# Kernel optimization log

Measured on AMD Instinct MI355X. Metric: run time of the kernel, lower is better.

Reference implementation:

```python
import jax, jax.numpy as jnp
import numpy as np
from jax import lax

K = 3  # AdaConv kernel_size inside conv_block


def conv2d(x, w, b, pad):
    # x: (B,C,H,W), w: (O,I,kh,kw) -> NCHW conv with symmetric padding
    y = lax.conv_general_dilated(x, w, (1, 1), [(pad, pad), (pad, pad)],
                                 dimension_numbers=('NCHW', 'OIHW', 'NCHW'))
    return y + b[None, :, None, None]


def unfold3(x):
    # nn.Unfold(kernel=3, pad=1): patches ordered channel-major then (kh,kw) row-major
    B, C, H, W = x.shape
    xp = jnp.pad(x, ((0, 0), (0, 0), (1, 1), (1, 1)))
    return jnp.stack([xp[:, :, i:i + H, j:j + W]
                      for i in range(K) for j in range(K)], axis=2)  # (B,C,9,H,W)


def adaconv(x, mask, aw_w, aw_b, mt_w, mt_b, c_w, c_b):
    # groups=1, groups_channels=out_ch in this configuration
    weight = conv2d(mask, aw_w, aw_b, pad=2)          # (B, 9, H, W)
    x = conv2d(x, c_w, c_b, pad=1)                    # (B, out_ch, H, W)
    p = unfold3(x)                                    # (B, out_ch, 9, H, W)
    out = jnp.einsum('bkhw,bckhw->bchw', weight, p)   # per-pixel adaptive conv
    mask2 = conv2d(mask, mt_w, mt_b, pad=2)
    return out, mask2


def lrelu(x):
    return jax.nn.leaky_relu(x, 0.01)


def setup_inputs() -> dict:
    key = jax.random.key(0)
    ks = jax.random.split(key, 20)
    B, Cin, Cout, Mi, Mo, H, W = 2, 64, 64, 64, 64, 256, 256
    s = 0.05
    d = {
        'x': jax.random.normal(ks[0], (B, Cin, H, W), jnp.float32),
        'mask': jax.random.normal(ks[1], (B, Mi, H, W), jnp.float32),
        # AdaConv 1 (in_ch->out_ch, mask_in->mask_out)
        'aw1_w': jax.random.normal(ks[2], (K * K, Mi, 2 * K - 1, 2 * K - 1), jnp.float32) * s,
        'aw1_b': jax.random.normal(ks[3], (K * K,), jnp.float32) * s,
        'mt1_w': jax.random.normal(ks[4], (Mo, Mi, 2 * K - 1, 2 * K - 1), jnp.float32) * s,
        'mt1_b': jax.random.normal(ks[5], (Mo,), jnp.float32) * s,
        'c1_w': jax.random.normal(ks[6], (Cout, Cin, K, K), jnp.float32) * s,
        'c1_b': jax.random.normal(ks[7], (Cout,), jnp.float32) * s,
        # AdaConv 2 (out_ch->out_ch, mask_out->mask_out)
        'aw2_w': jax.random.normal(ks[8], (K * K, Mo, 2 * K - 1, 2 * K - 1), jnp.float32) * s,
        'aw2_b': jax.random.normal(ks[9], (K * K,), jnp.float32) * s,
        'mt2_w': jax.random.normal(ks[10], (Mo, Mo, 2 * K - 1, 2 * K - 1), jnp.float32) * s,
        'mt2_b': jax.random.normal(ks[11], (Mo,), jnp.float32) * s,
        'c2_w': jax.random.normal(ks[12], (Cout, Cout, K, K), jnp.float32) * s,
        'c2_b': jax.random.normal(ks[13], (Cout,), jnp.float32) * s,
        # 1x1 residual conv
        'cr_w': jax.random.normal(ks[14], (Cout, Cin, 1, 1), jnp.float32) * s,
        'cr_b': jax.random.normal(ks[15], (Cout,), jnp.float32) * s,
    }
    return d


def reference(x, mask, aw1_w, aw1_b, mt1_w, mt1_b, c1_w, c1_b,
              aw2_w, aw2_b, mt2_w, mt2_b, c2_w, c2_b, cr_w, cr_b):
    res = conv2d(x, cr_w, cr_b, pad=0)
    x, mask = adaconv(x, mask, aw1_w, aw1_b, mt1_w, mt1_b, c1_w, c1_b)
    x, mask = lrelu(x), lrelu(mask)
    x, mask = adaconv(x, mask, aw2_w, aw2_b, mt2_w, mt2_b, c2_w, c2_b)
    x, mask = lrelu(x), lrelu(mask)
    return (x + res, mask)
```

## Files before the change

### kernel.cpp

```cpp
#include <hip/hip_runtime.h>

#define HWSZ 65536
#define CCH  64

typedef __bf16 bf16x8 __attribute__((ext_vector_type(8)));
typedef __bf16 bf16x4 __attribute__((ext_vector_type(4)));
typedef float  f32x4  __attribute__((ext_vector_type(4)));

__device__ inline void gload_lds16(const void* g, void* l) {
    __builtin_amdgcn_global_load_lds(
        (const __attribute__((address_space(1))) void*)g,
        (__attribute__((address_space(3))) void*)l, 16, 0, 0);
}


__device__ void cvt_body(int cb, const float* __restrict__ src,
                         __bf16* __restrict__ dst)
{
    int p  = cb * 256 + threadIdx.x;
    int b  = p >> 16, hw = p & 65535;
    const float* sp = src + (((size_t)b * 64) << 16) + hw;
    __bf16* dp = dst + (size_t)p * 64;
    #pragma unroll
    for (int c8 = 0; c8 < 8; ++c8) {
        bf16x8 v8;
        #pragma unroll
        for (int j = 0; j < 8; ++j)
            v8[j] = (__bf16)sp[(size_t)(c8 * 8 + j) << 16];
        *(bf16x8*)(dp + c8 * 8) = v8;
    }
}

__device__ void prep3_body(int cb, const float* __restrict__ src,
                           __bf16* __restrict__ dst)
{
    int t = cb * 256 + threadIdx.x;
    if (t >= 9 * 64 * 64) return;
    int j = t & 7;
    int u = (t >> 3) % 512;
    int k = t / 4096;
    int o = u >> 3;
    int s = (u & 7) ^ (o & 7);
    int i = s * 8 + j;
    dst[t] = (__bf16)src[((size_t)o * 64 + i) * 9 + k];
}

__device__ void prepF_body(int cb, const float* __restrict__ mt,
                           const float* __restrict__ aw, __bf16* __restrict__ dst)
{
    int t = cb * 256 + threadIdx.x;
    if (t >= 25 * 96 * 64) return;
    int j = t & 7;
    int u = (t >> 3) % 768;
    int k = t / 6144;
    int r = u >> 3;
    int s = (u & 7) ^ (r & 7);
    int i = s * 8 + j;
    float v = 0.f;
    if (r < 64)      v = mt[((size_t)r * 64 + i) * 25 + k];
    else if (r < 73) v = aw[((size_t)(r - 64) * 64 + i) * 25 + k];
    dst[t] = (__bf16)v;
}

__global__ __launch_bounds__(256) void k_prep(
    const float* x, const float* mask,
    const float* c1w, const float* c2w,
    const float* mt1w, const float* aw1w,
    const float* mt2w, const float* aw2w,
    __bf16* xh, __bf16* mh,
    __bf16* wbc1, __bf16* wbc2, __bf16* wbF1, __bf16* wbF2)
{
    int bid = blockIdx.x;
    if      (bid < 512)  cvt_body(bid, x, xh);
    else if (bid < 1024) cvt_body(bid - 512, mask, mh);
    else if (bid < 1168) prep3_body(bid - 1024, c1w, wbc1);
    else if (bid < 1312) prep3_body(bid - 1168, c2w, wbc2);
    else if (bid < 1912) prepF_body(bid - 1312, mt1w, aw1w, wbF1);
    else                 prepF_body(bid - 1912, mt2w, aw2w, wbF2);
}

template<int KSZ, int MFT, int RELU, int EPI>
__global__ __launch_bounds__(256) void k_mconv(
    const __bf16* __restrict__ xh, const __bf16* __restrict__ wb,
    const float* __restrict__ bias, const float* __restrict__ bias2,
    float* __restrict__ outf, __bf16* __restrict__ outh,
    float* __restrict__ out2)
{
    constexpr int PAD   = KSZ / 2;
    constexpr int TW    = 16 + 2 * PAD;
    constexpr int NPIX  = TW * TW;
    constexpr int KK    = KSZ * KSZ;
    constexpr int SROWS = (MFT == 5) ? 96 : 64;
    constexpr int SLICE = SROWS * 128;
    constexpr int NISS  = SROWS / 32;

    __shared__ __align__(16) __bf16 lx[NPIX * 64];
    __shared__ __align__(16) __bf16 lw[2][SROWS * 64];
    __shared__ float lb[80];

    const int t    = threadIdx.x;
    const int w0   = blockIdx.x * 16, h0 = blockIdx.y * 16, b = blockIdx.z;
    const int wvv  = t >> 6;
    const int lane = t & 63;
    const int px   = lane & 15;
    const int g    = lane >> 4;

    auto STAGE = [&](int k, int buf) {
        const char* gs = (const char*)wb + (size_t)k * SLICE;
        char* lbase = (char*)lw[buf];
        #pragma unroll
        for (int r = 0; r < NISS; ++r) {
            int ub = (wvv * NISS + r) * 64;
            gload_lds16(gs + (ub + lane) * 16, lbase + ub * 16);
        }
    };

    STAGE(0, 0);
    STAGE(1, 1);

    if (t < 64) lb[t] = bias[t];
    if constexpr (MFT == 5) {
        if (t >= 64 && t < 80) lb[t] = (t - 64 < 9) ? bias2[t - 64] : 0.f;
    }

    bf16x8 zv;
    #pragma unroll
    for (int j = 0; j < 8; ++j) zv[j] = (__bf16)0.f;
    constexpr int PITER = (NPIX + 255) / 256;
    #pragma unroll
    for (int pi = 0; pi < PITER; ++pi) {
        int pix = pi * 256 + t;
        if (pix < NPIX) {
            int sy = pix / TW, sx = pix - sy * TW;
            int gy = h0 + sy - PAD, gx = w0 + sx - PAD;
            bool ok = (unsigned)gy < 256u && (unsigned)gx < 256u;
            const __bf16* src = xh + ((((size_t)b << 16) + gy * 256 + gx) << 6);
            int rowbase = pix << 7, sw = (pix & 7) << 4;
            #pragma unroll
            for (int c8 = 0; c8 < 8; ++c8) {
                bf16x8 v8 = ok ? *(const bf16x8*)(src + c8 * 8) : zv;
                *(bf16x8*)((char*)lx + rowbase + ((c8 << 4) ^ sw)) = v8;
            }
        }
    }
    __syncthreads();

    f32x4 acc[MFT][4];
    #pragma unroll
    for (int m = 0; m < MFT; ++m)
        #pragma unroll
        for (int nf = 0; nf < 4; ++nf)
            acc[m][nf] = (f32x4){0.f, 0.f, 0.f, 0.f};

    #pragma unroll
    for (int k = 0; k < KK; ++k) {
        const __bf16* lwb = lw[k & 1];
        const int dy = k / KSZ, dx = k - dy * KSZ;

        bf16x8 bfr[4][2];
        #pragma unroll
        for (int nf = 0; nf < 4; ++nf) {
            int pix = (wvv * 4 + nf + dy) * TW + (px + dx);
            int rowbase = pix << 7, sw = (pix & 7) << 4;
            #pragma unroll
            for (int ks = 0; ks < 2; ++ks)
                bfr[nf][ks] = *(const bf16x8*)((const char*)lx + rowbase + ((((ks * 4 + g) << 4)) ^ sw));
        }
        bf16x8 afr[MFT][2];
        #pragma unroll
        for (int m = 0; m < MFT; ++m) {
            int o = m * 16 + px;
            int rowbase = o << 7, sw = (o & 7) << 4;
            #pragma unroll
            for (int ks = 0; ks < 2; ++ks)
                afr[m][ks] = *(const bf16x8*)((const char*)lwb + rowbase + ((((ks * 4 + g) << 4)) ^ sw));
        }
        __builtin_amdgcn_s_setprio(1);
        #pragma unroll
        for (int m = 0; m < MFT; ++m)
            #pragma unroll
            for (int nf = 0; nf < 4; ++nf)
                #pragma unroll
                for (int ks = 0; ks < 2; ++ks)
                    acc[m][nf] = __builtin_amdgcn_mfma_f32_16x16x32_bf16(
                        afr[m][ks], bfr[nf][ks], acc[m][nf], 0, 0, 0);
        __builtin_amdgcn_s_setprio(0);

        if (k == KK - 1) break;

        asm volatile("s_waitcnt lgkmcnt(0)" ::: "memory");
        __builtin_amdgcn_sched_barrier(0);
        __builtin_amdgcn_s_barrier();
        bool issued = (k + 2 < KK);
        if (issued) {
            STAGE(k + 2, k & 1);
            if constexpr (NISS == 2) asm volatile("s_waitcnt vmcnt(2)" ::: "memory");
            else                     asm volatile("s_waitcnt vmcnt(3)" ::: "memory");
        } else {
            asm volatile("s_waitcnt vmcnt(0)" ::: "memory");
        }
        __builtin_amdgcn_sched_barrier(0);
        __builtin_amdgcn_s_barrier();
    }

    #pragma unroll
    for (int m = 0; m < MFT; ++m) {
        #pragma unroll
        for (int nf = 0; nf < 4; ++nf) {
            int row = h0 + wvv * 4 + nf, col = w0 + px;
            if (m < 4) {
                float vj[4];
                #pragma unroll
                for (int j = 0; j < 4; ++j) {
                    float v = acc[m][nf][j] + lb[m * 16 + g * 4 + j];
                    if (RELU) v = v > 0.f ? v : 0.01f * v;
                    vj[j] = v;
                }
                if constexpr (EPI == 0) {
                    bf16x4 pk;
                    #pragma unroll
                    for (int j = 0; j < 4; ++j) pk[j] = (__bf16)vj[j];
                    *(bf16x4*)(outh + ((((size_t)b << 16) + row * 256 + col) << 6)
                                    + m * 16 + g * 4) = pk;
                } else {
                    #pragma unroll
                    for (int j = 0; j < 4; ++j)
                        outf[((size_t)(b * 64 + m * 16 + g * 4 + j) << 16)
                             + row * 256 + col] = vj[j];
                }
            } else {
                #pragma unroll
                for (int j = 0; j < 4; ++j) {
                    int o2 = g * 4 + j;
                    if (o2 < 9)
                        out2[((size_t)(b * 9 + o2) << 16) + row * 256 + col]
                            = acc[m][nf][j] + lb[64 + o2];
                }
            }
        }
    }
}

__global__ __launch_bounds__(256) void k_conv1x1(
    const __bf16* __restrict__ xh, const float* __restrict__ w,
    const float* __restrict__ bias, float* __restrict__ out)
{
    __shared__ __align__(16) float lwT[4096];
    __shared__ float lb[64];
    int t = threadIdx.x;
    for (int s = t; s < 4096; s += 256) lwT[s] = w[(s & 63) * 64 + (s >> 6)];
    if (t < 64) lb[t] = bias[t];
    __syncthreads();

    int p  = blockIdx.x * 256 + t;
    int b  = p >> 16, hw = p & 65535;
    const __bf16* xp = xh + (size_t)p * 64;

    float acc[64];
    #pragma unroll
    for (int o = 0; o < 64; ++o) acc[o] = lb[o];

    #pragma unroll
    for (int c8 = 0; c8 < 8; ++c8) {
        bf16x8 v8 = *(const bf16x8*)(xp + c8 * 8);
        #pragma unroll
        for (int j = 0; j < 8; ++j) {
            float xi = (float)v8[j];
            const float4* w4 = (const float4*)&lwT[(c8 * 8 + j) * 64];
            #pragma unroll
            for (int o4 = 0; o4 < 16; ++o4) {
                float4 wv = w4[o4];
                acc[o4*4+0] += wv.x * xi;
                acc[o4*4+1] += wv.y * xi;
                acc[o4*4+2] += wv.z * xi;
                acc[o4*4+3] += wv.w * xi;
            }
        }
    }
    float* op = out + (((size_t)b * 64) << 16) + hw;
    #pragma unroll
    for (int o = 0; o < 64; ++o) op[(size_t)o << 16] = acc[o];
}

__global__ __launch_bounds__(256, 4) void k_ada1(
    const float* __restrict__ wgt, const __bf16* __restrict__ xin,
    __bf16* __restrict__ outh)
{
    int t  = threadIdx.x;
    int pg = t >> 3, c8 = t & 7;
    int p  = blockIdx.x * 32 + pg;
    int b  = p >> 16, hw = p & 65535;
    int h  = hw >> 8, wc = hw & 255;

    const float* wp = wgt + ((size_t)(b * 9) << 16) + hw;
    const __bf16* cen = xin + (size_t)p * 64 + c8 * 8;

    float wk[9];
    const __bf16* nbp[9];
    #pragma unroll
    for (int dy = 0; dy < 3; ++dy)
        #pragma unroll
        for (int dx = 0; dx < 3; ++dx) {
            int k = dy * 3 + dx;
            bool ok = ((unsigned)(h + dy - 1) < 256u) &&
                      ((unsigned)(wc + dx - 1) < 256u);
            wk[k]  = ok ? wp[(size_t)k << 16] : 0.f;
            nbp[k] = ok ? cen + ((dy - 1) * 256 + (dx - 1)) * 64 : cen;
        }

    float acc[8] = {0.f,0.f,0.f,0.f,0.f,0.f,0.f,0.f};
    #pragma unroll
    for (int k = 0; k < 9; ++k) {
        bf16x8 v8 = *(const bf16x8*)nbp[k];
        float w = wk[k];
        #pragma unroll
        for (int j = 0; j < 8; ++j) acc[j] += w * (float)v8[j];
    }

    bf16x8 o8;
    #pragma unroll
    for (int j = 0; j < 8; ++j) {
        float v = acc[j];
        o8[j] = (__bf16)(v > 0.f ? v : 0.01f * v);
    }
    *(bf16x8*)(outh + (size_t)p * 64 + c8 * 8) = o8;
}

__global__ __launch_bounds__(256, 4) void k_ada2(
    const float* __restrict__ wgt, const __bf16* __restrict__ x2h,
    float* __restrict__ outf)
{
    __shared__ float ls[32 * 65];

    int t  = threadIdx.x;
    int pg = t >> 3, c8 = t & 7;
    int p  = blockIdx.x * 32 + pg;
    int b  = p >> 16, hw = p & 65535;
    int h  = hw >> 8, wc = hw & 255;

    const float* wp = wgt + ((size_t)(b * 9) << 16) + hw;
    const __bf16* cen = x2h + (size_t)p * 64 + c8 * 8;

    float wk[9];
    const __bf16* nbp[9];
    #pragma unroll
    for (int dy = 0; dy < 3; ++dy)
        #pragma unroll
        for (int dx = 0; dx < 3; ++dx) {
            int k = dy * 3 + dx;
            bool ok = ((unsigned)(h + dy - 1) < 256u) &&
                      ((unsigned)(wc + dx - 1) < 256u);
            wk[k]  = ok ? wp[(size_t)k << 16] : 0.f;
            nbp[k] = ok ? cen + ((dy - 1) * 256 + (dx - 1)) * 64 : cen;
        }

    float acc[8] = {0.f,0.f,0.f,0.f,0.f,0.f,0.f,0.f};
    #pragma unroll
    for (int k = 0; k < 9; ++k) {
        bf16x8 v8 = *(const bf16x8*)nbp[k];
        float w = wk[k];
        #pragma unroll
        for (int j = 0; j < 8; ++j) acc[j] += w * (float)v8[j];
    }

    #pragma unroll
    for (int j = 0; j < 8; ++j) {
        float v = acc[j];
        ls[pg * 65 + c8 * 8 + j] = v > 0.f ? v : 0.01f * v;
    }
    __syncthreads();

    int pbase = blockIdx.x * 32;
    int bb    = pbase >> 16, hwb = pbase & 65535;
    int pix   = t & 31, cq = t >> 5;
    #pragma unroll
    for (int i = 0; i < 8; ++i) {
        int c = i * 8 + cq;
        float v = ls[pix * 65 + c];
        float* op = outf + ((size_t)(bb * 64 + c) << 16) + hwb + pix;
        *op = *op + v;
    }
}

extern "C" void kernel_launch(void* const* d_in, const int* in_sizes, int n_in,
                              void* d_out, int out_size, void* d_ws, size_t ws_size,
                              hipStream_t stream)
{
    const float* x     = (const float*)d_in[0];
    const float* mask  = (const float*)d_in[1];
    const float* aw1_w = (const float*)d_in[2];
    const float* aw1_b = (const float*)d_in[3];
    const float* mt1_w = (const float*)d_in[4];
    const float* mt1_b = (const float*)d_in[5];
    const float* c1_w  = (const float*)d_in[6];
    const float* c1_b  = (const float*)d_in[7];
    const float* aw2_w = (const float*)d_in[8];
    const float* aw2_b = (const float*)d_in[9];
    const float* mt2_w = (const float*)d_in[10];
    const float* mt2_b = (const float*)d_in[11];
    const float* c2_w  = (const float*)d_in[12];
    const float* c2_b  = (const float*)d_in[13];
    const float* cr_w  = (const float*)d_in[14];
    const float* cr_b  = (const float*)d_in[15];

    float* out_x = (float*)d_out;
    float* out_m = (float*)d_out + 8388608;

    float*  wgt   = (float*)d_ws;
    __bf16* xh    = (__bf16*)((char*)d_ws + 4718592);
    __bf16* mh    = (__bf16*)((char*)d_ws + 21495808);
    __bf16* x2h   = mh;
    __bf16* wbase = (__bf16*)((char*)d_ws + 38273024);
    __bf16* wb_c1 = wbase;
    __bf16* wb_c2 = wbase + 36864;
    __bf16* wb_F1 = wbase + 73728;
    __bf16* wb_F2 = wbase + 227328;

    __bf16* maska_h = (__bf16*)out_x;
    __bf16* xa_h    = (__bf16*)out_x + 8388608;
    __bf16* x1_h    = (__bf16*)out_m;

    dim3 blk(256);
    dim3 gconv(16, 16, 2);
    dim3 gpix(512);
    dim3 gada(4096);

    k_prep<<<dim3(2512), blk, 0, stream>>>(x, mask, c1_w, c2_w,
        mt1_w, aw1_w, mt2_w, aw2_w, xh, mh, wb_c1, wb_c2, wb_F1, wb_F2);

    k_mconv<5,5,1,0><<<gconv, blk, 0, stream>>>(mh, wb_F1, mt1_b, aw1_b,
                                                nullptr, maska_h, wgt);
    k_mconv<3,4,0,0><<<gconv, blk, 0, stream>>>(xh, wb_c1, c1_b, nullptr,
                                                nullptr, x1_h, nullptr);
    k_ada1<<<gada, blk, 0, stream>>>(wgt, x1_h, xa_h);
    k_mconv<5,5,1,1><<<gconv, blk, 0, stream>>>(maska_h, wb_F2, mt2_b, aw2_b,
                                                out_m, nullptr, wgt);
    k_mconv<3,4,0,0><<<gconv, blk, 0, stream>>>(xa_h, wb_c2, c2_b, nullptr,
                                                nullptr, x2h, nullptr);
    k_conv1x1<<<gpix, blk, 0, stream>>>(xh, cr_w, cr_b, out_x);
    k_ada2<<<gada, blk, 0, stream>>>(wgt, x2h, out_x);
}
```

Baseline: 193.1 us.

## Split input channels into two halves to halve LDS tile footprint

The conv kernel now processes the 64 input channels in two 32-channel passes. It re-stages the input halo tile and the per-tap weight slices for each half, and the prep kernels repack weights into a matching [ci][k][row-pair] swizzled layout. This halves the shared-memory footprint for the input tile and weight buffers, which should let more blocks run per CU. The cost is twice as many pipeline barriers and tap iterations, an extra full-tile reload with its sync, and half as many MFMAs issued per tap iteration.

```diff
diff --git a/kernel.cpp b/kernel.cpp
--- a/kernel.cpp
+++ b/kernel.cpp
@@ -35,13 +35,16 @@
                            __bf16* __restrict__ dst)
 {
     int t = cb * 256 + threadIdx.x;
-    if (t >= 9 * 64 * 64) return;
-    int j = t & 7;
-    int u = (t >> 3) % 512;
-    int k = t / 4096;
-    int o = u >> 3;
-    int s = (u & 7) ^ (o & 7);
-    int i = s * 8 + j;
+    if (t >= 2 * 9 * 2048) return;
+    int j  = t & 7;
+    int u  = (t >> 3) & 255;
+    int q  = t >> 11;
+    int k  = q % 9, ci = q / 9;
+    int r  = u >> 3;
+    int v  = (u & 7) ^ (r & 7);
+    int o  = 2 * r + (v >> 2);
+    int g  = v & 3;
+    int i  = ci * 32 + g * 8 + j;
     dst[t] = (__bf16)src[((size_t)o * 64 + i) * 9 + k];
 }
 
@@ -49,17 +52,20 @@
                            const float* __restrict__ aw, __bf16* __restrict__ dst)
 {
     int t = cb * 256 + threadIdx.x;
-    if (t >= 25 * 96 * 64) return;
-    int j = t & 7;
-    int u = (t >> 3) % 768;
-    int k = t / 6144;
-    int r = u >> 3;
-    int s = (u & 7) ^ (r & 7);
-    int i = s * 8 + j;
-    float v = 0.f;
-    if (r < 64)      v = mt[((size_t)r * 64 + i) * 25 + k];
-    else if (r < 73) v = aw[((size_t)(r - 64) * 64 + i) * 25 + k];
-    dst[t] = (__bf16)v;
+    if (t >= 2 * 25 * 3072) return;
+    int j  = t & 7;
+    int u  = (t >> 3) % 384;
+    int q  = t / 3072;
+    int k  = q % 25, ci = q / 25;
+    int r  = u >> 3;
+    int v  = (u & 7) ^ (r & 7);
+    int o  = 2 * r + (v >> 2);
+    int g  = v & 3;
+    int i  = ci * 32 + g * 8 + j;
+    float val = 0.f;
+    if (o < 64)      val = mt[((size_t)o * 64 + i) * 25 + k];
+    else if (o < 73) val = aw[((size_t)(o - 64) * 64 + i) * 25 + k];
+    dst[t] = (__bf16)val;
 }
 
 __global__ __launch_bounds__(256) void k_prep(
@@ -91,11 +97,11 @@
     constexpr int NPIX  = TW * TW;
     constexpr int KK    = KSZ * KSZ;
     constexpr int SROWS = (MFT == 5) ? 96 : 64;
-    constexpr int SLICE = SROWS * 128;
-    constexpr int NISS  = SROWS / 32;
-
-    __shared__ __align__(16) __bf16 lx[NPIX * 64];
-    __shared__ __align__(16) __bf16 lw[2][SROWS * 64];
+    constexpr int SLICE = SROWS * 64;
+    constexpr int NPIX2 = NPIX / 2;
+
+    __shared__ __align__(16) __bf16 lx[NPIX2 * 64];
+    __shared__ __align__(16) __bf16 lw[2][SROWS * 32];
     __shared__ float lb[80];
 
     const int t    = threadIdx.x;
@@ -105,45 +111,22 @@
     const int px   = lane & 15;
     const int g    = lane >> 4;
 
-    auto STAGE = [&](int k, int buf) {
-        const char* gs = (const char*)wb + (size_t)k * SLICE;
+    auto STAGE = [&](int ci, int k, int buf) {
+        const char* gs = (const char*)wb + (size_t)(ci * KK + k) * SLICE;
         char* lbase = (char*)lw[buf];
-        #pragma unroll
-        for (int r = 0; r < NISS; ++r) {
-            int ub = (wvv * NISS + r) * 64;
+        if constexpr (MFT == 5) {
+            if (wvv < 3) {
+                #pragma unroll
+                for (int r = 0; r < 2; ++r) {
+                    int ub = wvv * 128 + r * 64;
+                    gload_lds16(gs + (ub + lane) * 16, lbase + ub * 16);
+                }
+            }
+        } else {
+            int ub = wvv * 64;
             gload_lds16(gs + (ub + lane) * 16, lbase + ub * 16);
         }
     };
-
-    STAGE(0, 0);
-    STAGE(1, 1);
-
-    if (t < 64) lb[t] = bias[t];
-    if constexpr (MFT == 5) {
-        if (t >= 64 && t < 80) lb[t] = (t - 64 < 9) ? bias2[t - 64] : 0.f;
-    }
-
-    bf16x8 zv;
-    #pragma unroll
-    for (int j = 0; j < 8; ++j) zv[j] = (__bf16)0.f;
-    constexpr int PITER = (NPIX + 255) / 256;
-    #pragma unroll
-    for (int pi = 0; pi < PITER; ++pi) {
-        int pix = pi * 256 + t;
-        if (pix < NPIX) {
-            int sy = pix / TW, sx = pix - sy * TW;
-            int gy = h0 + sy - PAD, gx = w0 + sx - PAD;
-            bool ok = (unsigned)gy < 256u && (unsigned)gx < 256u;
-            const __bf16* src = xh + ((((size_t)b << 16) + gy * 256 + gx) << 6);
-            int rowbase = pix << 7, sw = (pix & 7) << 4;
-            #pragma unroll
-            for (int c8 = 0; c8 < 8; ++c8) {
-                bf16x8 v8 = ok ? *(const bf16x8*)(src + c8 * 8) : zv;
-                *(bf16x8*)((char*)lx + rowbase + ((c8 << 4) ^ sw)) = v8;
-            }
-        }
-    }
-    __syncthreads();
 
     f32x4 acc[MFT][4];
     #pragma unroll
@@ -152,55 +135,87 @@
         for (int nf = 0; nf < 4; ++nf)
             acc[m][nf] = (f32x4){0.f, 0.f, 0.f, 0.f};
 
-    #pragma unroll
-    for (int k = 0; k < KK; ++k) {
-        const __bf16* lwb = lw[k & 1];
-        const int dy = k / KSZ, dx = k - dy * KSZ;
-
-        bf16x8 bfr[4][2];
-        #pragma unroll
-        for (int nf = 0; nf < 4; ++nf) {
-            int pix = (wvv * 4 + nf + dy) * TW + (px + dx);
-            int rowbase = pix << 7, sw = (pix & 7) << 4;
+    bf16x8 zv;
+    #pragma unroll
+    for (int j = 0; j < 8; ++j) zv[j] = (__bf16)0.f;
+
+    for (int ci = 0; ci < 2; ++ci) {
+        if (ci) __syncthreads();
+        STAGE(ci, 0, 0);
+        STAGE(ci, 1, 1);
+        if (ci == 0) {
+            if (t < 64) lb[t] = bias[t];
+            if constexpr (MFT == 5) {
+                if (t >= 64 && t < 80) lb[t] = (t - 64 < 9) ? bias2[t - 64] : 0.f;
+            }
+        }
+
+        constexpr int XITER = (NPIX * 4 + 255) / 256;
+        #pragma unroll
+        for (int xi = 0; xi < XITER; ++xi) {
+            int e = xi * 256 + t;
+            if (e < NPIX * 4) {
+                int pix = e >> 2, c4 = e & 3;
+                int sy = pix / TW, sx = pix - sy * TW;
+                int gy = h0 + sy - PAD, gx = w0 + sx - PAD;
+                bool ok = (unsigned)gy < 256u && (unsigned)gx < 256u;
+                bf16x8 v8 = zv;
+                if (ok) v8 = *(const bf16x8*)(xh + ((((size_t)b << 16) + gy * 256 + gx) << 6)
+                                              + ci * 32 + c4 * 8);
+                int row = pix >> 1;
+                int off = row * 128 + (((((pix & 1) << 2) + c4) ^ (row & 7)) << 4);
+                *(bf16x8*)((char*)lx + off) = v8;
+            }
+        }
+        __syncthreads();
+
+        #pragma unroll
+        for (int k = 0; k < KK; ++k) {
+            const __bf16* lwb = lw[k & 1];
+            const int dy = k / KSZ, dx = k - dy * KSZ;
+
+            bf16x8 bfr[4];
             #pragma unroll
-            for (int ks = 0; ks < 2; ++ks)
-                bfr[nf][ks] = *(const bf16x8*)((const char*)lx + rowbase + ((((ks * 4 + g) << 4)) ^ sw));
-        }
-        bf16x8 afr[MFT][2];
-        #pragma unroll
-        for (int m = 0; m < MFT; ++m) {
-            int o = m * 16 + px;
-            int rowbase = o << 7, sw = (o & 7) << 4;
+            for (int nf = 0; nf < 4; ++nf) {
+                int pix = (wvv * 4 + nf + dy) * TW + (px + dx);
+                int row = pix >> 1;
+                int off = row * 128 + (((((pix & 1) << 2) + g) ^ (row & 7)) << 4);
+                bfr[nf] = *(const bf16x8*)((const char*)lx + off);
+            }
+            bf16x8 afr[MFT];
             #pragma unroll
-            for (int ks = 0; ks < 2; ++ks)
-                afr[m][ks] = *(const bf16x8*)((const char*)lwb + rowbase + ((((ks * 4 + g) << 4)) ^ sw));
-        }
-        __builtin_amdgcn_s_setprio(1);
-        #pragma unroll
-        for (int m = 0; m < MFT; ++m)
+            for (int m = 0; m < MFT; ++m) {
+                int o = m * 16 + px;
+                int row = o >> 1;
+                int off = row * 128 + (((((o & 1) << 2) + g) ^ (row & 7)) << 4);
+                afr[m] = *(const bf16x8*)((const char*)lwb + off);
+            }
+            __builtin_amdgcn_s_setprio(1);
             #pragma unroll
-            for (int nf = 0; nf < 4; ++nf)
+            for (int m = 0; m < MFT; ++m)
                 #pragma unroll
-                for (int ks = 0; ks < 2; ++ks)
+                for (int nf = 0; nf < 4; ++nf)
                     acc[m][nf] = __builtin_amdgcn_mfma_f32_16x16x32_bf16(
-                        afr[m][ks], bfr[nf][ks], acc[m][nf], 0, 0, 0);
-        __builtin_amdgcn_s_setprio(0);
-
-        if (k == KK - 1) break;
-
-        asm volatile("s_waitcnt lgkmcnt(0)" ::: "memory");
-        __builtin_amdgcn_sched_barrier(0);
-        __builtin_amdgcn_s_barrier();
-        bool issued = (k + 2 < KK);
-        if (issued) {
-            STAGE(k + 2, k & 1);
-            if constexpr (NISS == 2) asm volatile("s_waitcnt vmcnt(2)" ::: "memory");
-            else                     asm volatile("s_waitcnt vmcnt(3)" ::: "memory");
-        } else {
-            asm volatile("s_waitcnt vmcnt(0)" ::: "memory");
-        }
-        __builtin_amdgcn_sched_barrier(0);
-        __builtin_amdgcn_s_barrier();
+                        afr[m], bfr[nf], acc[m][nf], 0, 0, 0);
+            __builtin_amdgcn_s_setprio(0);
+
+            if (k == KK - 1) break;
+
+            asm volatile("s_waitcnt lgkmcnt(0)" ::: "memory");
+            __builtin_amdgcn_sched_barrier(0);
+            __builtin_amdgcn_s_barrier();
+            bool issued = (k + 2 < KK);
+            if (issued) STAGE(ci, k + 2, k & 1);
+            if constexpr (MFT == 5) {
+                if (issued && wvv < 3) asm volatile("s_waitcnt vmcnt(2)" ::: "memory");
+                else                   asm volatile("s_waitcnt vmcnt(0)" ::: "memory");
+            } else {
+                if (issued) asm volatile("s_waitcnt vmcnt(1)" ::: "memory");
+                else        asm volatile("s_waitcnt vmcnt(0)" ::: "memory");
+            }
+            __builtin_amdgcn_sched_barrier(0);
+            __builtin_amdgcn_s_barrier();
+        }
     }
 
     #pragma unroll
```

Measured after the change: 196.9 us. Within noise of the previous version (+2.0%).
